# Kernel tuning notes

Measured on AMD Instinct MI355X. Metric: run time of the kernel, lower is better.

Reference implementation:

```python
import jax, jax.numpy as jnp
import numpy as np

FACTOR = 5

def _prob_attention(queries, keys, values):
    # queries/keys/values: [B, L, H, D]
    B, L_Q, H, D = queries.shape
    L_K = keys.shape[1]
    q = jnp.transpose(queries, (0, 2, 1, 3))  # [B,H,L_Q,D]
    k = jnp.transpose(keys, (0, 2, 1, 3))
    v = jnp.transpose(values, (0, 2, 1, 3))

    U_part = min(FACTOR * int(np.ceil(np.log(L_K))), L_K)  # sample_k
    u = min(FACTOR * int(np.ceil(np.log(L_Q))), L_Q)       # n_top

    # random K sampling (fixed key -> deterministic reference)
    skey = jax.random.key(42)
    index_sample = jax.random.randint(skey, (L_Q, U_part), 0, L_K)  # [L_Q, S]
    K_sample = k[:, :, index_sample, :]  # [B,H,L_Q,S,D]
    Q_K_sample = jnp.einsum('bhqd,bhqsd->bhqs', q, K_sample)  # [B,H,L_Q,S]

    # sparsity measure and top-u query selection
    M = jnp.max(Q_K_sample, axis=-1) - jnp.mean(Q_K_sample, axis=-1)  # [B,H,L_Q]
    _, M_top = jax.lax.top_k(M, u)  # [B,H,u]

    Q_reduce = jnp.take_along_axis(q, M_top[..., None], axis=2)  # [B,H,u,D]
    scores = jnp.einsum('bhud,bhkd->bhuk', Q_reduce, k)  # [B,H,u,L_K]
    scale = 1.0 / jnp.sqrt(jnp.asarray(D, dtype=q.dtype))
    scores = scores * scale

    # initial context: mean of V over keys, tiled over queries (mask_flag=False)
    V_mean = jnp.mean(v, axis=-2, keepdims=True)  # [B,H,1,D]
    context = jnp.broadcast_to(V_mean, (B, H, L_Q, D))

    attn = jax.nn.softmax(scores, axis=-1)  # [B,H,u,L_K]
    update = jnp.einsum('bhuk,bhkd->bhud', attn, v)  # [B,H,u,D]

    # scatter updates into context at selected query positions
    bi = jnp.arange(B)[:, None, None]
    hi = jnp.arange(H)[None, :, None]
    context = context.at[bi, hi, M_top].set(update)

    return jnp.transpose(context, (0, 2, 1, 3))  # [B,L_Q,H,D]


def setup_inputs() -> dict:
    key = jax.random.key(0)
    kq, kk, kv = jax.random.split(key, 3)
    B, L, H, D = 4, 2048, 8, 64
    return {
        'queries': jax.random.normal(kq, (B, L, H, D), dtype=jnp.float32),
        'keys': jax.random.normal(kk, (B, L, H, D), dtype=jnp.float32),
        'values': jax.random.normal(kv, (B, L, H, D), dtype=jnp.float32),
        'attn_mask': jnp.zeros((1,), dtype=jnp.bool_),  # unused (mask_flag=False)
    }


def reference(queries, keys, values, attn_mask):
    context = _prob_attention(queries, keys, values)
    return context
```

## Files before the change

kernel.cpp:

```cpp
#include <hip/hip_runtime.h>
#include <hip/hip_bf16.h>
#include <math.h>
#include <stdint.h>

static constexpr int BB = 4;
static constexpr int LL = 2048;
static constexpr int HH = 8;
static constexpr int DD = 64;
static constexpr int UU = 40;
static constexpr int NSAMP = 40;
static constexpr int BHL = BB * HH * LL;
static constexpr int NIDX = LL * NSAMP;
static constexpr int ROWSTRIDE = HH * DD;
static constexpr int VCHUNKS = 64;
static constexpr int NC = 16;
static constexpr int CROWS = LL / NC;
static constexpr int NBLK = BB * HH * NC;

static constexpr size_t WS_NEED = 5420032;

__device__ __forceinline__ uint32_t rotl32(uint32_t x, uint32_t n) {
  return (x << n) | (x >> (32u - n));
}

__device__ __forceinline__ void tf2x32(uint32_t k0, uint32_t k1,
                                       uint32_t x0, uint32_t x1,
                                       uint32_t& o0, uint32_t& o1) {
  uint32_t ks[3] = {k0, k1, k0 ^ k1 ^ 0x1BD11BDAu};
  x0 += ks[0];
  x1 += ks[1];
  const uint32_t rotA[4] = {13u, 15u, 26u, 6u};
  const uint32_t rotB[4] = {17u, 29u, 16u, 24u};
#pragma unroll
  for (int i = 0; i < 5; ++i) {
    const uint32_t* r = (i & 1) ? rotB : rotA;
#pragma unroll
    for (int j = 0; j < 4; ++j) {
      x0 += x1;
      x1 = rotl32(x1, r[j]);
      x1 ^= x0;
    }
    x0 += ks[(i + 1) % 3];
    x1 += ks[(i + 2) % 3] + (uint32_t)(i + 1);
  }
  o0 = x0;
  o1 = x1;
}

__global__ void k_build_idx(int* __restrict__ idx) {
  int i = blockIdx.x * 256 + threadIdx.x;
  if (i >= NIDX) return;
  uint32_t ka, kb;
  tf2x32(0u, 42u, 0u, 1u, ka, kb);
  uint32_t o0, o1;
  tf2x32(ka, kb, 0u, (uint32_t)i, o0, o1);
  idx[i] = (int)((o0 ^ o1) & 2047u);
}

__device__ __forceinline__ float dot4(float4 a, float4 b) {
  return a.x * b.x + a.y * b.y + a.z * b.z + a.w * b.w;
}

__global__ void k_scores_M(const float* __restrict__ q, const float* __restrict__ k,
                           const int* __restrict__ idx, float* __restrict__ M) {
  int w = (blockIdx.x * blockDim.x + threadIdx.x) >> 6;
  int lane = threadIdx.x & 63;
  if (w >= BHL) return;
  int qq = w & (LL - 1);
  int h = (w >> 11) & (HH - 1);
  int b = w >> 14;
  int rr = lane >> 3;
  int dc = lane & 7;
  const float* qrow = q + (((size_t)b * LL + qq) * HH + h) * DD;
  float4 q0 = ((const float4*)qrow)[dc * 2];
  float4 q1 = ((const float4*)qrow)[dc * 2 + 1];
  const float* kbase = k + ((size_t)b * LL * HH + h) * DD;
  const int* ridx = idx + qq * NSAMP;
  int kr[5];
#pragma unroll
  for (int it = 0; it < 5; ++it) kr[it] = ridx[it * 8 + rr];
  float mx = -1.0e30f, sm = 0.0f;
#pragma unroll
  for (int it = 0; it < 5; ++it) {
    const float4* kp = (const float4*)(kbase + (size_t)kr[it] * ROWSTRIDE);
    float p = dot4(q0, kp[dc * 2]) + dot4(q1, kp[dc * 2 + 1]);
    p += __shfl_xor(p, 1);
    p += __shfl_xor(p, 2);
    p += __shfl_xor(p, 4);
    mx = fmaxf(mx, p);
    sm += p;
  }
#pragma unroll
  for (int off = 8; off <= 32; off <<= 1) {
    mx = fmaxf(mx, __shfl_xor(mx, off));
    sm += __shfl_xor(sm, off);
  }
  if (lane == 0) M[w] = mx - sm * (1.0f / (float)NSAMP);
}

__global__ void k_topk(const float* __restrict__ M, int* __restrict__ mtop) {
  __shared__ uint32_t keys[LL];
  __shared__ int hist[256];
  __shared__ int scan_res[2];
  __shared__ int nsel, neq;
  __shared__ int sel[UU];
  __shared__ int eqlist[64];
  int bh = blockIdx.x;
  int t = threadIdx.x;
  const float* m = M + (size_t)bh * LL;
  for (int i = t; i < LL; i += 256) {
    uint32_t u = __float_as_uint(m[i]);
    keys[i] = (u & 0x80000000u) ? ~u : (u | 0x80000000u);
  }
  if (t == 0) { nsel = 0; neq = 0; }
  __syncthreads();

  uint32_t prefix = 0, prefmask = 0;
  int remaining = UU;
#pragma unroll
  for (int shift = 24; shift >= 0; shift -= 8) {
    hist[t] = 0;
    __syncthreads();
    for (int i = t; i < LL; i += 256) {
      uint32_t kk = keys[i];
      if ((kk & prefmask) == prefix) atomicAdd(&hist[(kk >> shift) & 0xFF], 1);
    }
    __syncthreads();
    if (t < 64) {
      int b0 = t * 4;
      int c0 = hist[b0], c1 = hist[b0 + 1], c2 = hist[b0 + 2], c3 = hist[b0 + 3];
      int g = c0 + c1 + c2 + c3;
      int s = g;
#pragma unroll
      for (int off = 1; off < 64; off <<= 1) {
        int o = __shfl_down(s, off);
        if (t + off < 64) s += o;
      }
      int a3 = s - g;
      int a2 = a3 + c3;
      int a1 = a2 + c2;
      int a0 = a1 + c1;
      if (a3 < remaining && remaining <= a3 + c3) { scan_res[0] = b0 + 3; scan_res[1] = a3; }
      if (a2 < remaining && remaining <= a2 + c2) { scan_res[0] = b0 + 2; scan_res[1] = a2; }
      if (a1 < remaining && remaining <= a1 + c1) { scan_res[0] = b0 + 1; scan_res[1] = a1; }
      if (a0 < remaining && remaining <= a0 + c0) { scan_res[0] = b0 + 0; scan_res[1] = a0; }
    }
    __syncthreads();
    prefix |= ((uint32_t)scan_res[0] << shift);
    prefmask |= (0xFFu << shift);
    remaining -= scan_res[1];
    __syncthreads();
  }

  uint32_t T = prefix;
  for (int i = t; i < LL; i += 256) {
    uint32_t kk = keys[i];
    if (kk > T) {
      int p = atomicAdd(&nsel, 1);
      sel[p] = i;
    } else if (kk == T) {
      int p = atomicAdd(&neq, 1);
      if (p < 64) eqlist[p] = i;
    }
  }
  __syncthreads();
  if (t == 0) {
    int need = UU - nsel;
    int count = neq < 64 ? neq : 64;
    for (int r = 0; r < need; ++r) {
      int mn = 1 << 30, mpos = 0;
      for (int e = 0; e < count; ++e)
        if (eqlist[e] < mn) { mn = eqlist[e]; mpos = e; }
      sel[nsel + r] = mn;
      eqlist[mpos] = 1 << 30;
    }
  }
  __syncthreads();
  if (t < UU) mtop[bh * UU + t] = sel[t];
}

__global__ void k_vmean_part(const float* __restrict__ v, float* __restrict__ partial) {
  __shared__ float part[4][DD];
  int bid = blockIdx.x;
  int bh = bid >> 6;
  int chunk = bid & 63;
  int b = bh >> 3, h = bh & 7;
  int t = threadIdx.x;
  int wv = t >> 6, lane = t & 63;
  int l0 = chunk * (LL / VCHUNKS);
  const float* base = v + ((size_t)b * LL * HH + h) * DD + lane;
  float s = 0.0f;
#pragma unroll
  for (int r = wv; r < LL / VCHUNKS; r += 4) s += base[(size_t)(l0 + r) * ROWSTRIDE];
  part[wv][lane] = s;
  __syncthreads();
  if (t < DD) {
    partial[(size_t)bid * DD + t] =
        (part[0][t] + part[1][t]) + (part[2][t] + part[3][t]);
  }
}

__global__ void k_vmean_final(const float* __restrict__ partial, float* __restrict__ vmean) {
  int bh = blockIdx.x;
  int d = threadIdx.x;
  const float* p = partial + (size_t)bh * VCHUNKS * DD + d;
  float s = 0.0f;
#pragma unroll
  for (int c = 0; c < VCHUNKS; ++c) s += p[(size_t)c * DD];
  vmean[bh * DD + d] = s * (1.0f / (float)LL);
}

__global__ void k_fill(const float* __restrict__ vmean, float* __restrict__ out) {
  int f = blockIdx.x * 256 + threadIdx.x;
  int d4 = f & 15;
  int h = (f >> 4) & 7;
  int b = f >> 18;
  ((float4*)out)[f] = ((const float4*)vmean)[(((b << 3) + h) << 4) + d4];
}

__global__ void __launch_bounds__(256)
k_attn_part(const float* __restrict__ q, const float* __restrict__ k,
            const float* __restrict__ v, const int* __restrict__ mtop,
            float* __restrict__ pm, float* __restrict__ ps,
            float* __restrict__ pacc) {
  __shared__ float qs[UU][DD];
  __shared__ float sc[UU][CROWS];
  int blk = blockIdx.x;
  int c = blk & (NC - 1);
  int bh = blk >> 4;
  int b = bh >> 3, h = bh & 7;
  int t = threadIdx.x;
  int wv = t >> 6, lane = t & 63;
  int l0 = c * CROWS;

  for (int i = t; i < UU * DD; i += 256) {
    int j = i >> 6, d = i & 63;
    int l = mtop[bh * UU + j];
    qs[j][d] = q[(((size_t)b * LL + l) * HH + h) * DD + d];
  }
  __syncthreads();

  const float* kbase = k + ((size_t)b * LL * HH + h) * DD;

  int rr = lane & 15, dcq = lane >> 4;
  float4 kv0[4], kv1[4];
  {
    const float* kr0 = kbase + (size_t)(l0 + wv * 32 + rr) * ROWSTRIDE + dcq * 16;
    const float* kr1 = kbase + (size_t)(l0 + wv * 32 + 16 + rr) * ROWSTRIDE + dcq * 16;
#pragma unroll
    for (int i = 0; i < 4; ++i) {
      kv0[i] = *(const float4*)(kr0 + i * 4);
      kv1[i] = *(const float4*)(kr1 + i * 4);
    }
  }
#pragma unroll 4
  for (int j = 0; j < UU; ++j) {
    const float* qp = &qs[j][dcq * 16];
    float4 qa = *(const float4*)(qp);
    float4 qb = *(const float4*)(qp + 4);
    float4 qc = *(const float4*)(qp + 8);
    float4 qd = *(const float4*)(qp + 12);
    float p0 = dot4(qa, kv0[0]) + dot4(qb, kv0[1]) + dot4(qc, kv0[2]) + dot4(qd, kv0[3]);
    float p1 = dot4(qa, kv1[0]) + dot4(qb, kv1[1]) + dot4(qc, kv1[2]) + dot4(qd, kv1[3]);
    p0 += __shfl_xor(p0, 16);
    p0 += __shfl_xor(p0, 32);
    p1 += __shfl_xor(p1, 16);
    p1 += __shfl_xor(p1, 32);
    if (lane < 16) {
      sc[j][wv * 32 + lane] = p0 * 0.125f;
      sc[j][wv * 32 + 16 + lane] = p1 * 0.125f;
    }
  }
  __syncthreads();

#pragma unroll
  for (int jj = 0; jj < 10; ++jj) {
    int j = wv * 10 + jj;
    float a0 = sc[j][lane];
    float a1 = sc[j][lane + 64];
    float mx = fmaxf(a0, a1);
#pragma unroll
    for (int off = 32; off; off >>= 1) mx = fmaxf(mx, __shfl_xor(mx, off));
    float e0 = expf(a0 - mx), e1 = expf(a1 - mx);
    sc[j][lane] = e0;
    sc[j][lane + 64] = e1;
    float s = e0 + e1;
#pragma unroll
    for (int off = 32; off; off >>= 1) s += __shfl_xor(s, off);
    if (lane == 0) {
      pm[(size_t)blk * UU + j] = mx;
      ps[(size_t)blk * UU + j] = s;
    }
  }

  const float* vbase = v + ((size_t)b * LL * HH + h) * DD + lane;
  float acc[10];
#pragma unroll
  for (int jj = 0; jj < 10; ++jj) acc[jj] = 0.0f;
  for (int r = 0; r < CROWS; r += 4) {
    float v0 = vbase[(size_t)(l0 + r + 0) * ROWSTRIDE];
    float v1 = vbase[(size_t)(l0 + r + 1) * ROWSTRIDE];
    float v2 = vbase[(size_t)(l0 + r + 2) * ROWSTRIDE];
    float v3 = vbase[(size_t)(l0 + r + 3) * ROWSTRIDE];
#pragma unroll
    for (int jj = 0; jj < 10; ++jj) {
      int j = wv * 10 + jj;
      float4 p4 = *(const float4*)&sc[j][r];
      acc[jj] += p4.x * v0 + p4.y * v1 + p4.z * v2 + p4.w * v3;
    }
  }
#pragma unroll
  for (int jj = 0; jj < 10; ++jj) {
    int j = wv * 10 + jj;
    pacc[((size_t)blk * UU + j) * DD + lane] = acc[jj];
  }
}

__global__ void k_attn_comb(const float* __restrict__ pm, const float* __restrict__ ps,
                            const float* __restrict__ pacc, const int* __restrict__ mtop,
                            float* __restrict__ out) {
  int wid = (blockIdx.x * 256 + threadIdx.x) >> 6;
  int lane = threadIdx.x & 63;
  if (wid >= BB * HH * UU) return;
  int j = wid % UU;
  int bh = wid / UU;
  int b = bh >> 3, h = bh & 7;
  float mv = (lane < NC) ? pm[((size_t)(bh * NC + lane)) * UU + j] : -1.0e30f;
  float mx = mv;
#pragma unroll
  for (int off = 8; off; off >>= 1) mx = fmaxf(mx, __shfl_xor(mx, off));
  mx = __shfl(mx, 0);
  float e = (lane < NC) ? expf(mv - mx) : 0.0f;
  float sv = (lane < NC) ? ps[((size_t)(bh * NC + lane)) * UU + j] * e : 0.0f;
  float st = sv;
#pragma unroll
  for (int off = 8; off; off >>= 1) st += __shfl_xor(st, off);
  st = __shfl(st, 0);
  float a = 0.0f;
#pragma unroll
  for (int c = 0; c < NC; ++c) {
    float ec = __shfl(e, c);
    a += ec * pacc[((size_t)(bh * NC + c) * UU + j) * DD + lane];
  }
  int l = mtop[bh * UU + j];
  out[(((size_t)b * LL + l) * HH + h) * DD + lane] = a / st;
}

__global__ void k_attn_mono(const float* __restrict__ q, const float* __restrict__ k,
                            const float* __restrict__ v, const int* __restrict__ mtop,
                            float* __restrict__ out) {
  __shared__ float sc[LL];
  __shared__ float redm[4];
  __shared__ float reds[4];
  __shared__ float redp[4][DD];
  int blk = blockIdx.x;
  int j = blk % UU;
  int bh = blk / UU;
  int b = bh >> 3, h = bh & 7;
  int l = mtop[bh * UU + j];
  int t = threadIdx.x;
  int wv = t >> 6, lane = t & 63;
  int dc = t & 15, r2 = (t >> 4) & 3;
  const float4* qrow = (const float4*)(q + (((size_t)b * LL + l) * HH + h) * DD);
  float4 qv = qrow[dc];
  const float* kbase = k + ((size_t)b * LL * HH + h) * DD;
#pragma unroll 4
  for (int base = wv * 4; base < LL; base += 16) {
    int row = base + r2;
    const float4* krow = (const float4*)(kbase + (size_t)row * ROWSTRIDE);
    float4 kv = krow[dc];
    float p = dot4(qv, kv);
    p += __shfl_xor(p, 1);
    p += __shfl_xor(p, 2);
    p += __shfl_xor(p, 4);
    p += __shfl_xor(p, 8);
    if (dc == 0) sc[row] = p * 0.125f;
  }
  __syncthreads();
  const float4* sc4 = (const float4*)sc;
  float4 ea0 = sc4[t];
  float4 ea1 = sc4[t + 256];
  float mx = fmaxf(fmaxf(fmaxf(ea0.x, ea0.y), fmaxf(ea0.z, ea0.w)),
                   fmaxf(fmaxf(ea1.x, ea1.y), fmaxf(ea1.z, ea1.w)));
#pragma unroll
  for (int off = 32; off; off >>= 1) mx = fmaxf(mx, __shfl_xor(mx, off));
  if (lane == 0) redm[wv] = mx;
  __syncthreads();
  mx = fmaxf(fmaxf(redm[0], redm[1]), fmaxf(redm[2], redm[3]));
  ea0.x = expf(ea0.x - mx); ea0.y = expf(ea0.y - mx);
  ea0.z = expf(ea0.z - mx); ea0.w = expf(ea0.w - mx);
  ea1.x = expf(ea1.x - mx); ea1.y = expf(ea1.y - mx);
  ea1.z = expf(ea1.z - mx); ea1.w = expf(ea1.w - mx);
  float psum = ((ea0.x + ea0.y) + (ea0.z + ea0.w)) + ((ea1.x + ea1.y) + (ea1.z + ea1.w));
  float4* sc4w = (float4*)sc;
  sc4w[t] = ea0;
  sc4w[t + 256] = ea1;
#pragma unroll
  for (int off = 32; off; off >>= 1) psum += __shfl_xor(psum, off);
  if (lane == 0) reds[wv] = psum;
  __syncthreads();
  float inv = 1.0f / ((reds[0] + reds[1]) + (reds[2] + reds[3]));
  const float* vbase = v + ((size_t)b * LL * HH + h) * DD + lane;
  float acc = 0.0f;
#pragma unroll 2
  for (int base = wv * 4; base < LL; base += 16) {
    float4 p4 = sc4[base >> 2];
    acc += p4.x * vbase[(size_t)(base + 0) * ROWSTRIDE];
    acc += p4.y * vbase[(size_t)(base + 1) * ROWSTRIDE];
    acc += p4.z * vbase[(size_t)(base + 2) * ROWSTRIDE];
    acc += p4.w * vbase[(size_t)(base + 3) * ROWSTRIDE];
  }
  redp[wv][lane] = acc;
  __syncthreads();
  if (t < DD) {
    float r = (redp[0][t] + redp[1][t]) + (redp[2][t] + redp[3][t]);
    out[(((size_t)b * LL + l) * HH + h) * DD + t] = r * inv;
  }
}

extern "C" void kernel_launch(void* const* d_in, const int* in_sizes, int n_in,
                              void* d_out, int out_size, void* d_ws, size_t ws_size,
                              hipStream_t stream) {
  const float* q = (const float*)d_in[0];
  const float* k = (const float*)d_in[1];
  const float* v = (const float*)d_in[2];
  float* out = (float*)d_out;
  char* ws = (char*)d_ws;
  bool big = ws_size >= WS_NEED;

  if (big) {
    float* pm = (float*)(ws);
    float* ps = (float*)(ws + 81920);
    float* pacc = (float*)(ws + 163840);
    float* M = (float*)(ws);
    int* idx = (int*)(ws + 262144);
    float* vpart = (float*)(ws);
    int* mtop = (int*)(ws + 5406720);
    float* vmean = (float*)(ws + 5411840);

    k_build_idx<<<(NIDX + 255) / 256, 256, 0, stream>>>(idx);
    k_scores_M<<<BHL / 4, 256, 0, stream>>>(q, k, idx, M);
    k_topk<<<BB * HH, 256, 0, stream>>>(M, mtop);
    k_vmean_part<<<BB * HH * VCHUNKS, 256, 0, stream>>>(v, vpart);
    k_vmean_final<<<BB * HH, DD, 0, stream>>>(vpart, vmean);
    k_fill<<<(BB * LL * HH * DD / 4) / 256, 256, 0, stream>>>(vmean, out);
    k_attn_part<<<NBLK, 256, 0, stream>>>(q, k, v, mtop, pm, ps, pacc);
    k_attn_comb<<<(BB * HH * UU * 64) / 256, 256, 0, stream>>>(pm, ps, pacc, mtop, out);
  } else {
    float* M = (float*)(ws);
    int* idx = (int*)(ws + 262144);
    int* mtop = (int*)(ws + 589824);
    float* vmean = (float*)(ws + 594944);
    float* vpart = (float*)(ws);

    k_build_idx<<<(NIDX + 255) / 256, 256, 0, stream>>>(idx);
    k_scores_M<<<BHL / 4, 256, 0, stream>>>(q, k, idx, M);
    k_topk<<<BB * HH, 256, 0, stream>>>(M, mtop);
    k_vmean_part<<<BB * HH * VCHUNKS, 256, 0, stream>>>(v, vpart);
    k_vmean_final<<<BB * HH, DD, 0, stream>>>(vpart, vmean);
    k_fill<<<(BB * LL * HH * DD / 4) / 256, 256, 0, stream>>>(vmean, out);
    k_attn_mono<<<BB * HH * UU, 256, 0, stream>>>(q, k, v, mtop, out);
  }
}
```

Before: 178.6 us.

## Fuse random index generation into sampling kernel and double attention key split

The Threefry index generation moves into k_scores_M, with each lane computing one sample index that is then shuffled across the wave. This removes a separate launch and the idx buffer round-trip. Blocks in k_scores_M are also remapped in a strided order. The split-K attention now uses 32 chunks of 64 keys instead of 16 chunks of 128, giving more blocks at the cost of more partials to combine. The workspace requirement roughly doubles, so the big path depends on the workspace size provided.

```diff
diff --git a/kernel.cpp b/kernel.cpp
--- a/kernel.cpp
+++ b/kernel.cpp
@@ -10,14 +10,13 @@
 static constexpr int UU = 40;
 static constexpr int NSAMP = 40;
 static constexpr int BHL = BB * HH * LL;
-static constexpr int NIDX = LL * NSAMP;
 static constexpr int ROWSTRIDE = HH * DD;
 static constexpr int VCHUNKS = 64;
-static constexpr int NC = 16;
+static constexpr int NC = 32;
 static constexpr int CROWS = LL / NC;
 static constexpr int NBLK = BB * HH * NC;
 
-static constexpr size_t WS_NEED = 5420032;
+static constexpr size_t WS_NEED = 10826752;
 
 __device__ __forceinline__ uint32_t rotl32(uint32_t x, uint32_t n) {
   return (x << n) | (x >> (32u - n));
@@ -47,38 +46,35 @@
   o1 = x1;
 }
 
-__global__ void k_build_idx(int* __restrict__ idx) {
-  int i = blockIdx.x * 256 + threadIdx.x;
-  if (i >= NIDX) return;
+__device__ __forceinline__ float dot4(float4 a, float4 b) {
+  return a.x * b.x + a.y * b.y + a.z * b.z + a.w * b.w;
+}
+
+__global__ void k_scores_M(const float* __restrict__ q, const float* __restrict__ k,
+                           float* __restrict__ M) {
+  const int NWG = BHL / 4;
+  int wg = (blockIdx.x & 7) * (NWG / 8) + (blockIdx.x >> 3);
+  int w = wg * 4 + (threadIdx.x >> 6);
+  int lane = threadIdx.x & 63;
+  int qq = w & (LL - 1);
+  int h = (w >> 11) & (HH - 1);
+  int b = w >> 14;
+
   uint32_t ka, kb;
   tf2x32(0u, 42u, 0u, 1u, ka, kb);
   uint32_t o0, o1;
-  tf2x32(ka, kb, 0u, (uint32_t)i, o0, o1);
-  idx[i] = (int)((o0 ^ o1) & 2047u);
-}
-
-__device__ __forceinline__ float dot4(float4 a, float4 b) {
-  return a.x * b.x + a.y * b.y + a.z * b.z + a.w * b.w;
-}
-
-__global__ void k_scores_M(const float* __restrict__ q, const float* __restrict__ k,
-                           const int* __restrict__ idx, float* __restrict__ M) {
-  int w = (blockIdx.x * blockDim.x + threadIdx.x) >> 6;
-  int lane = threadIdx.x & 63;
-  if (w >= BHL) return;
-  int qq = w & (LL - 1);
-  int h = (w >> 11) & (HH - 1);
-  int b = w >> 14;
+  tf2x32(ka, kb, 0u, (uint32_t)(qq * NSAMP + lane), o0, o1);
+  int idxv = (int)((o0 ^ o1) & 2047u);
+
   int rr = lane >> 3;
   int dc = lane & 7;
   const float* qrow = q + (((size_t)b * LL + qq) * HH + h) * DD;
   float4 q0 = ((const float4*)qrow)[dc * 2];
   float4 q1 = ((const float4*)qrow)[dc * 2 + 1];
   const float* kbase = k + ((size_t)b * LL * HH + h) * DD;
-  const int* ridx = idx + qq * NSAMP;
   int kr[5];
 #pragma unroll
-  for (int it = 0; it < 5; ++it) kr[it] = ridx[it * 8 + rr];
+  for (int it = 0; it < 5; ++it) kr[it] = __shfl(idxv, it * 8 + rr);
   float mx = -1.0e30f, sm = 0.0f;
 #pragma unroll
   for (int it = 0; it < 5; ++it) {
@@ -227,7 +223,7 @@
   __shared__ float sc[UU][CROWS];
   int blk = blockIdx.x;
   int c = blk & (NC - 1);
-  int bh = blk >> 4;
+  int bh = blk >> 5;
   int b = bh >> 3, h = bh & 7;
   int t = threadIdx.x;
   int wv = t >> 6, lane = t & 63;
@@ -243,15 +239,11 @@
   const float* kbase = k + ((size_t)b * LL * HH + h) * DD;
 
   int rr = lane & 15, dcq = lane >> 4;
-  float4 kv0[4], kv1[4];
+  float4 kv0[4];
   {
-    const float* kr0 = kbase + (size_t)(l0 + wv * 32 + rr) * ROWSTRIDE + dcq * 16;
-    const float* kr1 = kbase + (size_t)(l0 + wv * 32 + 16 + rr) * ROWSTRIDE + dcq * 16;
-#pragma unroll
-    for (int i = 0; i < 4; ++i) {
-      kv0[i] = *(const float4*)(kr0 + i * 4);
-      kv1[i] = *(const float4*)(kr1 + i * 4);
-    }
+    const float* kr0 = kbase + (size_t)(l0 + wv * 16 + rr) * ROWSTRIDE + dcq * 16;
+#pragma unroll
+    for (int i = 0; i < 4; ++i) kv0[i] = *(const float4*)(kr0 + i * 4);
   }
 #pragma unroll 4
   for (int j = 0; j < UU; ++j) {
@@ -261,15 +253,9 @@
     float4 qc = *(const float4*)(qp + 8);
     float4 qd = *(const float4*)(qp + 12);
     float p0 = dot4(qa, kv0[0]) + dot4(qb, kv0[1]) + dot4(qc, kv0[2]) + dot4(qd, kv0[3]);
-    float p1 = dot4(qa, kv1[0]) + dot4(qb, kv1[1]) + dot4(qc, kv1[2]) + dot4(qd, kv1[3]);
     p0 += __shfl_xor(p0, 16);
     p0 += __shfl_xor(p0, 32);
-    p1 += __shfl_xor(p1, 16);
-    p1 += __shfl_xor(p1, 32);
-    if (lane < 16) {
-      sc[j][wv * 32 + lane] = p0 * 0.125f;
-      sc[j][wv * 32 + 16 + lane] = p1 * 0.125f;
-    }
+    if (lane < 16) sc[j][wv * 16 + lane] = p0 * 0.125f;
   }
   __syncthreads();
 
@@ -277,14 +263,12 @@
   for (int jj = 0; jj < 10; ++jj) {
     int j = wv * 10 + jj;
     float a0 = sc[j][lane];
-    float a1 = sc[j][lane + 64];
-    float mx = fmaxf(a0, a1);
+    float mx = a0;
 #pragma unroll
     for (int off = 32; off; off >>= 1) mx = fmaxf(mx, __shfl_xor(mx, off));
-    float e0 = expf(a0 - mx), e1 = expf(a1 - mx);
+    float e0 = expf(a0 - mx);
     sc[j][lane] = e0;
-    sc[j][lane + 64] = e1;
-    float s = e0 + e1;
+    float s = e0;
 #pragma unroll
     for (int off = 32; off; off >>= 1) s += __shfl_xor(s, off);
     if (lane == 0) {
@@ -328,13 +312,13 @@
   float mv = (lane < NC) ? pm[((size_t)(bh * NC + lane)) * UU + j] : -1.0e30f;
   float mx = mv;
 #pragma unroll
-  for (int off = 8; off; off >>= 1) mx = fmaxf(mx, __shfl_xor(mx, off));
+  for (int off = 16; off; off >>= 1) mx = fmaxf(mx, __shfl_xor(mx, off));
   mx = __shfl(mx, 0);
   float e = (lane < NC) ? expf(mv - mx) : 0.0f;
   float sv = (lane < NC) ? ps[((size_t)(bh * NC + lane)) * UU + j] * e : 0.0f;
   float st = sv;
 #pragma unroll
-  for (int off = 8; off; off >>= 1) st += __shfl_xor(st, off);
+  for (int off = 16; off; off >>= 1) st += __shfl_xor(st, off);
   st = __shfl(st, 0);
   float a = 0.0f;
 #pragma unroll
@@ -430,16 +414,14 @@
 
   if (big) {
     float* pm = (float*)(ws);
-    float* ps = (float*)(ws + 81920);
-    float* pacc = (float*)(ws + 163840);
+    float* ps = (float*)(ws + 163840);
+    float* pacc = (float*)(ws + 327680);
     float* M = (float*)(ws);
-    int* idx = (int*)(ws + 262144);
     float* vpart = (float*)(ws);
-    int* mtop = (int*)(ws + 5406720);
-    float* vmean = (float*)(ws + 5411840);
-
-    k_build_idx<<<(NIDX + 255) / 256, 256, 0, stream>>>(idx);
-    k_scores_M<<<BHL / 4, 256, 0, stream>>>(q, k, idx, M);
+    int* mtop = (int*)(ws + 10813440);
+    float* vmean = (float*)(ws + 10818560);
+
+    k_scores_M<<<BHL / 4, 256, 0, stream>>>(q, k, M);
     k_topk<<<BB * HH, 256, 0, stream>>>(M, mtop);
     k_vmean_part<<<BB * HH * VCHUNKS, 256, 0, stream>>>(v, vpart);
     k_vmean_final<<<BB * HH, DD, 0, stream>>>(vpart, vmean);
@@ -448,13 +430,11 @@
     k_attn_comb<<<(BB * HH * UU * 64) / 256, 256, 0, stream>>>(pm, ps, pacc, mtop, out);
   } else {
     float* M = (float*)(ws);
-    int* idx = (int*)(ws + 262144);
-    int* mtop = (int*)(ws + 589824);
-    float* vmean = (float*)(ws + 594944);
     float* vpart = (float*)(ws);
-
-    k_build_idx<<<(NIDX + 255) / 256, 256, 0, stream>>>(idx);
-    k_scores_M<<<BHL / 4, 256, 0, stream>>>(q, k, idx, M);
+    int* mtop = (int*)(ws + 524288);
+    float* vmean = (float*)(ws + 529408);
+
+    k_scores_M<<<BHL / 4, 256, 0, stream>>>(q, k, M);
     k_topk<<<BB * HH, 256, 0, stream>>>(M, mtop);
     k_vmean_part<<<BB * HH * VCHUNKS, 256, 0, stream>>>(v, vpart);
     k_vmean_final<<<BB * HH, DD, 0, stream>>>(vpart, vmean);
```

Result: no change. 177.2 us (-0.8%).

## Fuse pipeline into four kernels with inline index RNG and lookup-table output

Applied to the files above, without the earlier changes.

The sample-index generation is computed inline in the scoring kernel, with indices shared through wave shuffles and K loads batched ahead of the math. The V partial means are produced in the same launch as scoring. Top-k and the final V-mean reduction share one launch, and top-k also writes a per-position lookup table. The attention partial kernel is split into two query halves to double block count. The fill and combine kernels become a single output kernel that writes either the V mean or the combined attention row per position. This cuts launch count and the extra full-output write pass. The cost is redundant threefry work per wave and extra table memory traffic.

```diff
diff --git a/kernel.cpp b/kernel.cpp
--- a/kernel.cpp
+++ b/kernel.cpp
@@ -10,14 +10,15 @@
 static constexpr int UU = 40;
 static constexpr int NSAMP = 40;
 static constexpr int BHL = BB * HH * LL;
-static constexpr int NIDX = LL * NSAMP;
 static constexpr int ROWSTRIDE = HH * DD;
 static constexpr int VCHUNKS = 64;
 static constexpr int NC = 16;
-static constexpr int CROWS = LL / NC;
-static constexpr int NBLK = BB * HH * NC;
-
-static constexpr size_t WS_NEED = 5420032;
+static constexpr int CR = 128;
+static constexpr int QS = 20;
+static constexpr int SCOREBLK = BHL / 4;
+static constexpr int P1BLK = SCOREBLK + BB * HH * VCHUNKS;
+
+static constexpr size_t WS_NEED = 5682176;
 
 __device__ __forceinline__ uint32_t rotl32(uint32_t x, uint32_t n) {
   return (x << n) | (x >> (32u - n));
@@ -47,175 +48,177 @@
   o1 = x1;
 }
 
-__global__ void k_build_idx(int* __restrict__ idx) {
-  int i = blockIdx.x * 256 + threadIdx.x;
-  if (i >= NIDX) return;
-  uint32_t ka, kb;
-  tf2x32(0u, 42u, 0u, 1u, ka, kb);
-  uint32_t o0, o1;
-  tf2x32(ka, kb, 0u, (uint32_t)i, o0, o1);
-  idx[i] = (int)((o0 ^ o1) & 2047u);
-}
-
 __device__ __forceinline__ float dot4(float4 a, float4 b) {
   return a.x * b.x + a.y * b.y + a.z * b.z + a.w * b.w;
 }
 
-__global__ void k_scores_M(const float* __restrict__ q, const float* __restrict__ k,
-                           const int* __restrict__ idx, float* __restrict__ M) {
-  int w = (blockIdx.x * blockDim.x + threadIdx.x) >> 6;
-  int lane = threadIdx.x & 63;
-  if (w >= BHL) return;
-  int qq = w & (LL - 1);
-  int h = (w >> 11) & (HH - 1);
-  int b = w >> 14;
-  int rr = lane >> 3;
-  int dc = lane & 7;
-  const float* qrow = q + (((size_t)b * LL + qq) * HH + h) * DD;
-  float4 q0 = ((const float4*)qrow)[dc * 2];
-  float4 q1 = ((const float4*)qrow)[dc * 2 + 1];
-  const float* kbase = k + ((size_t)b * LL * HH + h) * DD;
-  const int* ridx = idx + qq * NSAMP;
-  int kr[5];
-#pragma unroll
-  for (int it = 0; it < 5; ++it) kr[it] = ridx[it * 8 + rr];
-  float mx = -1.0e30f, sm = 0.0f;
-#pragma unroll
-  for (int it = 0; it < 5; ++it) {
-    const float4* kp = (const float4*)(kbase + (size_t)kr[it] * ROWSTRIDE);
-    float p = dot4(q0, kp[dc * 2]) + dot4(q1, kp[dc * 2 + 1]);
-    p += __shfl_xor(p, 1);
-    p += __shfl_xor(p, 2);
-    p += __shfl_xor(p, 4);
-    mx = fmaxf(mx, p);
-    sm += p;
-  }
-#pragma unroll
-  for (int off = 8; off <= 32; off <<= 1) {
-    mx = fmaxf(mx, __shfl_xor(mx, off));
-    sm += __shfl_xor(sm, off);
-  }
-  if (lane == 0) M[w] = mx - sm * (1.0f / (float)NSAMP);
-}
-
-__global__ void k_topk(const float* __restrict__ M, int* __restrict__ mtop) {
-  __shared__ uint32_t keys[LL];
-  __shared__ int hist[256];
-  __shared__ int scan_res[2];
-  __shared__ int nsel, neq;
-  __shared__ int sel[UU];
-  __shared__ int eqlist[64];
-  int bh = blockIdx.x;
-  int t = threadIdx.x;
-  const float* m = M + (size_t)bh * LL;
-  for (int i = t; i < LL; i += 256) {
-    uint32_t u = __float_as_uint(m[i]);
-    keys[i] = (u & 0x80000000u) ? ~u : (u | 0x80000000u);
-  }
-  if (t == 0) { nsel = 0; neq = 0; }
-  __syncthreads();
-
-  uint32_t prefix = 0, prefmask = 0;
-  int remaining = UU;
-#pragma unroll
-  for (int shift = 24; shift >= 0; shift -= 8) {
-    hist[t] = 0;
+__global__ void __launch_bounds__(256)
+k_phase1(const float* __restrict__ q, const float* __restrict__ k,
+         const float* __restrict__ v, float* __restrict__ M,
+         float* __restrict__ vpart) {
+  if (blockIdx.x < SCOREBLK) {
+    int wg = (blockIdx.x & 7) * (SCOREBLK / 8) + (blockIdx.x >> 3);
+    int w = wg * 4 + (threadIdx.x >> 6);
+    int lane = threadIdx.x & 63;
+    int qq = w & (LL - 1);
+    int h = (w >> 11) & (HH - 1);
+    int b = w >> 14;
+    uint32_t ka, kb;
+    tf2x32(0u, 42u, 0u, 1u, ka, kb);
+    uint32_t o0, o1;
+    tf2x32(ka, kb, 0u, (uint32_t)(qq * NSAMP + lane), o0, o1);
+    int idxv = (int)((o0 ^ o1) & 2047u);
+    int rr = lane >> 3;
+    int dc = lane & 7;
+    const float* qrow = q + (((size_t)b * LL + qq) * HH + h) * DD;
+    float4 q0 = ((const float4*)qrow)[dc * 2];
+    float4 q1 = ((const float4*)qrow)[dc * 2 + 1];
+    const float* kbase = k + ((size_t)b * LL * HH + h) * DD;
+    int kr[5];
+#pragma unroll
+    for (int it = 0; it < 5; ++it) kr[it] = __shfl(idxv, it * 8 + rr);
+    float4 kva[5], kvb[5];
+#pragma unroll
+    for (int it = 0; it < 5; ++it) {
+      const float4* kp = (const float4*)(kbase + (size_t)kr[it] * ROWSTRIDE);
+      kva[it] = kp[dc * 2];
+      kvb[it] = kp[dc * 2 + 1];
+    }
+    float mx = -1.0e30f, sm = 0.0f;
+#pragma unroll
+    for (int it = 0; it < 5; ++it) {
+      float p = dot4(q0, kva[it]) + dot4(q1, kvb[it]);
+      p += __shfl_xor(p, 1);
+      p += __shfl_xor(p, 2);
+      p += __shfl_xor(p, 4);
+      mx = fmaxf(mx, p);
+      sm += p;
+    }
+#pragma unroll
+    for (int off = 8; off <= 32; off <<= 1) {
+      mx = fmaxf(mx, __shfl_xor(mx, off));
+      sm += __shfl_xor(sm, off);
+    }
+    if (lane == 0) M[w] = mx - sm * (1.0f / (float)NSAMP);
+  } else {
+    __shared__ float part[4][DD];
+    int bid = blockIdx.x - SCOREBLK;
+    int bh = bid >> 6;
+    int chunk = bid & 63;
+    int b = bh >> 3, h = bh & 7;
+    int t = threadIdx.x;
+    int wv = t >> 6, lane = t & 63;
+    int l0 = chunk * (LL / VCHUNKS);
+    const float* base = v + ((size_t)b * LL * HH + h) * DD + lane;
+    float s = 0.0f;
+#pragma unroll
+    for (int r = wv; r < LL / VCHUNKS; r += 4) s += base[(size_t)(l0 + r) * ROWSTRIDE];
+    part[wv][lane] = s;
     __syncthreads();
+    if (t < DD) {
+      vpart[(size_t)bid * DD + t] =
+          (part[0][t] + part[1][t]) + (part[2][t] + part[3][t]);
+    }
+  }
+}
+
+__global__ void __launch_bounds__(256)
+k_phase2(const float* __restrict__ M, const float* __restrict__ vpart,
+         int* __restrict__ mtop, float* __restrict__ vmean, int* __restrict__ tbl) {
+  if (blockIdx.x < BB * HH) {
+    __shared__ uint32_t keys[LL];
+    __shared__ int hist[256];
+    __shared__ int scan_res[2];
+    __shared__ int nsel, neq;
+    __shared__ int sel[UU];
+    __shared__ int eqlist[64];
+    int bh = blockIdx.x;
+    int t = threadIdx.x;
+    const float* m = M + (size_t)bh * LL;
+    for (int i = t; i < LL; i += 256) {
+      uint32_t u = __float_as_uint(m[i]);
+      keys[i] = (u & 0x80000000u) ? ~u : (u | 0x80000000u);
+      tbl[bh * LL + i] = -1;
+    }
+    if (t == 0) { nsel = 0; neq = 0; }
+    __syncthreads();
+
+    uint32_t prefix = 0, prefmask = 0;
+    int remaining = UU;
+#pragma unroll
+    for (int shift = 24; shift >= 0; shift -= 8) {
+      hist[t] = 0;
+      __syncthreads();
+      for (int i = t; i < LL; i += 256) {
+        uint32_t kk = keys[i];
+        if ((kk & prefmask) == prefix) atomicAdd(&hist[(kk >> shift) & 0xFF], 1);
+      }
+      __syncthreads();
+      if (t < 64) {
+        int b0 = t * 4;
+        int c0 = hist[b0], c1 = hist[b0 + 1], c2 = hist[b0 + 2], c3 = hist[b0 + 3];
+        int g = c0 + c1 + c2 + c3;
+        int s = g;
+#pragma unroll
+        for (int off = 1; off < 64; off <<= 1) {
+          int o = __shfl_down(s, off);
+          if (t + off < 64) s += o;
+        }
+        int a3 = s - g;
+        int a2 = a3 + c3;
+        int a1 = a2 + c2;
+        int a0 = a1 + c1;
+        if (a3 < remaining && remaining <= a3 + c3) { scan_res[0] = b0 + 3; scan_res[1] = a3; }
+        if (a2 < remaining && remaining <= a2 + c2) { scan_res[0] = b0 + 2; scan_res[1] = a2; }
+        if (a1 < remaining && remaining <= a1 + c1) { scan_res[0] = b0 + 1; scan_res[1] = a1; }
+        if (a0 < remaining && remaining <= a0 + c0) { scan_res[0] = b0 + 0; scan_res[1] = a0; }
+      }
+      __syncthreads();
+      prefix |= ((uint32_t)scan_res[0] << shift);
+      prefmask |= (0xFFu << shift);
+      remaining -= scan_res[1];
+      __syncthreads();
+    }
+
+    uint32_t T = prefix;
     for (int i = t; i < LL; i += 256) {
       uint32_t kk = keys[i];
-      if ((kk & prefmask) == prefix) atomicAdd(&hist[(kk >> shift) & 0xFF], 1);
+      if (kk > T) {
+        int p = atomicAdd(&nsel, 1);
+        sel[p] = i;
+      } else if (kk == T) {
+        int p = atomicAdd(&neq, 1);
+        if (p < 64) eqlist[p] = i;
+      }
     }
     __syncthreads();
-    if (t < 64) {
-      int b0 = t * 4;
-      int c0 = hist[b0], c1 = hist[b0 + 1], c2 = hist[b0 + 2], c3 = hist[b0 + 3];
-      int g = c0 + c1 + c2 + c3;
-      int s = g;
-#pragma unroll
-      for (int off = 1; off < 64; off <<= 1) {
-        int o = __shfl_down(s, off);
-        if (t + off < 64) s += o;
+    if (t == 0) {
+      int need = UU - nsel;
+      int count = neq < 64 ? neq : 64;
+      for (int r = 0; r < need; ++r) {
+        int mn = 1 << 30, mpos = 0;
+        for (int e = 0; e < count; ++e)
+          if (eqlist[e] < mn) { mn = eqlist[e]; mpos = e; }
+        sel[nsel + r] = mn;
+        eqlist[mpos] = 1 << 30;
       }
-      int a3 = s - g;
-      int a2 = a3 + c3;
-      int a1 = a2 + c2;
-      int a0 = a1 + c1;
-      if (a3 < remaining && remaining <= a3 + c3) { scan_res[0] = b0 + 3; scan_res[1] = a3; }
-      if (a2 < remaining && remaining <= a2 + c2) { scan_res[0] = b0 + 2; scan_res[1] = a2; }
-      if (a1 < remaining && remaining <= a1 + c1) { scan_res[0] = b0 + 1; scan_res[1] = a1; }
-      if (a0 < remaining && remaining <= a0 + c0) { scan_res[0] = b0 + 0; scan_res[1] = a0; }
     }
     __syncthreads();
-    prefix |= ((uint32_t)scan_res[0] << shift);
-    prefmask |= (0xFFu << shift);
-    remaining -= scan_res[1];
-    __syncthreads();
-  }
-
-  uint32_t T = prefix;
-  for (int i = t; i < LL; i += 256) {
-    uint32_t kk = keys[i];
-    if (kk > T) {
-      int p = atomicAdd(&nsel, 1);
-      sel[p] = i;
-    } else if (kk == T) {
-      int p = atomicAdd(&neq, 1);
-      if (p < 64) eqlist[p] = i;
-    }
-  }
-  __syncthreads();
-  if (t == 0) {
-    int need = UU - nsel;
-    int count = neq < 64 ? neq : 64;
-    for (int r = 0; r < need; ++r) {
-      int mn = 1 << 30, mpos = 0;
-      for (int e = 0; e < count; ++e)
-        if (eqlist[e] < mn) { mn = eqlist[e]; mpos = e; }
-      sel[nsel + r] = mn;
-      eqlist[mpos] = 1 << 30;
-    }
-  }
-  __syncthreads();
-  if (t < UU) mtop[bh * UU + t] = sel[t];
-}
-
-__global__ void k_vmean_part(const float* __restrict__ v, float* __restrict__ partial) {
-  __shared__ float part[4][DD];
-  int bid = blockIdx.x;
-  int bh = bid >> 6;
-  int chunk = bid & 63;
-  int b = bh >> 3, h = bh & 7;
-  int t = threadIdx.x;
-  int wv = t >> 6, lane = t & 63;
-  int l0 = chunk * (LL / VCHUNKS);
-  const float* base = v + ((size_t)b * LL * HH + h) * DD + lane;
-  float s = 0.0f;
-#pragma unroll
-  for (int r = wv; r < LL / VCHUNKS; r += 4) s += base[(size_t)(l0 + r) * ROWSTRIDE];
-  part[wv][lane] = s;
-  __syncthreads();
-  if (t < DD) {
-    partial[(size_t)bid * DD + t] =
-        (part[0][t] + part[1][t]) + (part[2][t] + part[3][t]);
-  }
-}
-
-__global__ void k_vmean_final(const float* __restrict__ partial, float* __restrict__ vmean) {
-  int bh = blockIdx.x;
-  int d = threadIdx.x;
-  const float* p = partial + (size_t)bh * VCHUNKS * DD + d;
-  float s = 0.0f;
-#pragma unroll
-  for (int c = 0; c < VCHUNKS; ++c) s += p[(size_t)c * DD];
-  vmean[bh * DD + d] = s * (1.0f / (float)LL);
-}
-
-__global__ void k_fill(const float* __restrict__ vmean, float* __restrict__ out) {
-  int f = blockIdx.x * 256 + threadIdx.x;
-  int d4 = f & 15;
-  int h = (f >> 4) & 7;
-  int b = f >> 18;
-  ((float4*)out)[f] = ((const float4*)vmean)[(((b << 3) + h) << 4) + d4];
+    if (t < UU) {
+      mtop[bh * UU + t] = sel[t];
+      tbl[bh * LL + sel[t]] = t;
+    }
+  } else {
+    int bh = blockIdx.x - BB * HH;
+    int d = threadIdx.x;
+    if (d < DD) {
+      const float* p = vpart + (size_t)bh * VCHUNKS * DD + d;
+      float s = 0.0f;
+#pragma unroll
+      for (int c = 0; c < VCHUNKS; ++c) s += p[(size_t)c * DD];
+      vmean[bh * DD + d] = s * (1.0f / (float)LL);
+    }
+  }
 }
 
 __global__ void __launch_bounds__(256)
@@ -223,25 +226,26 @@
             const float* __restrict__ v, const int* __restrict__ mtop,
             float* __restrict__ pm, float* __restrict__ ps,
             float* __restrict__ pacc) {
-  __shared__ float qs[UU][DD];
-  __shared__ float sc[UU][CROWS];
+  __shared__ float qs_[QS][DD];
+  __shared__ float sc[QS][CR];
   int blk = blockIdx.x;
   int c = blk & (NC - 1);
-  int bh = blk >> 4;
+  int qh = (blk >> 4) & 1;
+  int bh = blk >> 5;
   int b = bh >> 3, h = bh & 7;
   int t = threadIdx.x;
   int wv = t >> 6, lane = t & 63;
-  int l0 = c * CROWS;
-
-  for (int i = t; i < UU * DD; i += 256) {
-    int j = i >> 6, d = i & 63;
-    int l = mtop[bh * UU + j];
-    qs[j][d] = q[(((size_t)b * LL + l) * HH + h) * DD + d];
+  int l0 = c * CR;
+  int j0 = qh * QS;
+
+  for (int i = t; i < QS * DD; i += 256) {
+    int jj = i >> 6, d = i & 63;
+    int l = mtop[bh * UU + j0 + jj];
+    qs_[jj][d] = q[(((size_t)b * LL + l) * HH + h) * DD + d];
   }
   __syncthreads();
 
   const float* kbase = k + ((size_t)b * LL * HH + h) * DD;
-
   int rr = lane & 15, dcq = lane >> 4;
   float4 kv0[4], kv1[4];
   {
@@ -254,8 +258,8 @@
     }
   }
 #pragma unroll 4
-  for (int j = 0; j < UU; ++j) {
-    const float* qp = &qs[j][dcq * 16];
+  for (int jj = 0; jj < QS; ++jj) {
+    const float* qp = &qs_[jj][dcq * 16];
     float4 qa = *(const float4*)(qp);
     float4 qb = *(const float4*)(qp + 4);
     float4 qc = *(const float4*)(qp + 8);
@@ -267,83 +271,89 @@
     p1 += __shfl_xor(p1, 16);
     p1 += __shfl_xor(p1, 32);
     if (lane < 16) {
-      sc[j][wv * 32 + lane] = p0 * 0.125f;
-      sc[j][wv * 32 + 16 + lane] = p1 * 0.125f;
-    }
-  }
-  __syncthreads();
-
-#pragma unroll
-  for (int jj = 0; jj < 10; ++jj) {
-    int j = wv * 10 + jj;
-    float a0 = sc[j][lane];
-    float a1 = sc[j][lane + 64];
+      sc[jj][wv * 32 + lane] = p0 * 0.125f;
+      sc[jj][wv * 32 + 16 + lane] = p1 * 0.125f;
+    }
+  }
+  __syncthreads();
+
+#pragma unroll
+  for (int u = 0; u < 5; ++u) {
+    int jj = wv * 5 + u;
+    float a0 = sc[jj][lane];
+    float a1 = sc[jj][lane + 64];
     float mx = fmaxf(a0, a1);
 #pragma unroll
     for (int off = 32; off; off >>= 1) mx = fmaxf(mx, __shfl_xor(mx, off));
     float e0 = expf(a0 - mx), e1 = expf(a1 - mx);
-    sc[j][lane] = e0;
-    sc[j][lane + 64] = e1;
+    sc[jj][lane] = e0;
+    sc[jj][lane + 64] = e1;
     float s = e0 + e1;
 #pragma unroll
     for (int off = 32; off; off >>= 1) s += __shfl_xor(s, off);
     if (lane == 0) {
-      pm[(size_t)blk * UU + j] = mx;
-      ps[(size_t)blk * UU + j] = s;
-    }
-  }
-
+      pm[(size_t)(bh * NC + c) * UU + j0 + jj] = mx;
+      ps[(size_t)(bh * NC + c) * UU + j0 + jj] = s;
+    }
+  }
   const float* vbase = v + ((size_t)b * LL * HH + h) * DD + lane;
-  float acc[10];
-#pragma unroll
-  for (int jj = 0; jj < 10; ++jj) acc[jj] = 0.0f;
-  for (int r = 0; r < CROWS; r += 4) {
+  float acc[5] = {0.f, 0.f, 0.f, 0.f, 0.f};
+  for (int r = 0; r < CR; r += 4) {
     float v0 = vbase[(size_t)(l0 + r + 0) * ROWSTRIDE];
     float v1 = vbase[(size_t)(l0 + r + 1) * ROWSTRIDE];
     float v2 = vbase[(size_t)(l0 + r + 2) * ROWSTRIDE];
     float v3 = vbase[(size_t)(l0 + r + 3) * ROWSTRIDE];
 #pragma unroll
-    for (int jj = 0; jj < 10; ++jj) {
-      int j = wv * 10 + jj;
-      float4 p4 = *(const float4*)&sc[j][r];
-      acc[jj] += p4.x * v0 + p4.y * v1 + p4.z * v2 + p4.w * v3;
-    }
-  }
-#pragma unroll
-  for (int jj = 0; jj < 10; ++jj) {
-    int j = wv * 10 + jj;
-    pacc[((size_t)blk * UU + j) * DD + lane] = acc[jj];
-  }
-}
-
-__global__ void k_attn_comb(const float* __restrict__ pm, const float* __restrict__ ps,
-                            const float* __restrict__ pacc, const int* __restrict__ mtop,
-                            float* __restrict__ out) {
+    for (int u = 0; u < 5; ++u) {
+      float4 p4 = *(const float4*)&sc[wv * 5 + u][r];
+      acc[u] += p4.x * v0 + p4.y * v1 + p4.z * v2 + p4.w * v3;
+    }
+  }
+#pragma unroll
+  for (int u = 0; u < 5; ++u) {
+    pacc[((size_t)(bh * NC + c) * UU + j0 + wv * 5 + u) * DD + lane] = acc[u];
+  }
+}
+
+__global__ void __launch_bounds__(256)
+k_out(const float* __restrict__ pm, const float* __restrict__ ps,
+      const float* __restrict__ pacc, const int* __restrict__ tbl,
+      const float* __restrict__ vmean, float* __restrict__ out) {
   int wid = (blockIdx.x * 256 + threadIdx.x) >> 6;
   int lane = threadIdx.x & 63;
-  if (wid >= BB * HH * UU) return;
-  int j = wid % UU;
-  int bh = wid / UU;
+  int l = wid & (LL - 1);
+  int bh = wid >> 11;
   int b = bh >> 3, h = bh & 7;
-  float mv = (lane < NC) ? pm[((size_t)(bh * NC + lane)) * UU + j] : -1.0e30f;
-  float mx = mv;
-#pragma unroll
-  for (int off = 8; off; off >>= 1) mx = fmaxf(mx, __shfl_xor(mx, off));
-  mx = __shfl(mx, 0);
-  float e = (lane < NC) ? expf(mv - mx) : 0.0f;
-  float sv = (lane < NC) ? ps[((size_t)(bh * NC + lane)) * UU + j] * e : 0.0f;
-  float st = sv;
-#pragma unroll
-  for (int off = 8; off; off >>= 1) st += __shfl_xor(st, off);
-  st = __shfl(st, 0);
-  float a = 0.0f;
-#pragma unroll
-  for (int c = 0; c < NC; ++c) {
-    float ec = __shfl(e, c);
-    a += ec * pacc[((size_t)(bh * NC + c) * UU + j) * DD + lane];
-  }
-  int l = mtop[bh * UU + j];
-  out[(((size_t)b * LL + l) * HH + h) * DD + lane] = a / st;
+  int j = tbl[bh * LL + l];
+  float* orow = out + (((size_t)b * LL + l) * HH + h) * DD;
+  if (j < 0) {
+    orow[lane] = vmean[bh * DD + lane];
+  } else {
+    float mv = (lane < NC) ? pm[(size_t)(bh * NC + lane) * UU + j] : -1.0e30f;
+    float mx = mv;
+#pragma unroll
+    for (int off = 32; off; off >>= 1) mx = fmaxf(mx, __shfl_xor(mx, off));
+    float e = (lane < NC) ? expf(mv - mx) : 0.0f;
+    float sv = (lane < NC) ? ps[(size_t)(bh * NC + lane) * UU + j] * e : 0.0f;
+    float st = sv;
+#pragma unroll
+    for (int off = 32; off; off >>= 1) st += __shfl_xor(st, off);
+    float a = 0.0f;
+#pragma unroll
+    for (int c2 = 0; c2 < NC; ++c2) {
+      float ec = __shfl(e, c2);
+      a += ec * pacc[((size_t)(bh * NC + c2) * UU + j) * DD + lane];
+    }
+    orow[lane] = a / st;
+  }
+}
+
+__global__ void k_fill(const float* __restrict__ vmean, float* __restrict__ out) {
+  int f = blockIdx.x * 256 + threadIdx.x;
+  int d4 = f & 15;
+  int h = (f >> 4) & 7;
+  int b = f >> 18;
+  ((float4*)out)[f] = ((const float4*)vmean)[(((b << 3) + h) << 4) + d4];
 }
 
 __global__ void k_attn_mono(const float* __restrict__ q, const float* __restrict__ k,
@@ -426,38 +436,30 @@
   const float* v = (const float*)d_in[2];
   float* out = (float*)d_out;
   char* ws = (char*)d_ws;
-  bool big = ws_size >= WS_NEED;
-
-  if (big) {
+
+  if (ws_size >= WS_NEED) {
+    float* M = (float*)(ws);
+    float* vpart = (float*)(ws + 262144);
     float* pm = (float*)(ws);
     float* ps = (float*)(ws + 81920);
     float* pacc = (float*)(ws + 163840);
-    float* M = (float*)(ws);
-    int* idx = (int*)(ws + 262144);
-    float* vpart = (float*)(ws);
     int* mtop = (int*)(ws + 5406720);
     float* vmean = (float*)(ws + 5411840);
-
-    k_build_idx<<<(NIDX + 255) / 256, 256, 0, stream>>>(idx);
-    k_scores_M<<<BHL / 4, 256, 0, stream>>>(q, k, idx, M);
-    k_topk<<<BB * HH, 256, 0, stream>>>(M, mtop);
-    k_vmean_part<<<BB * HH * VCHUNKS, 256, 0, stream>>>(v, vpart);
-    k_vmean_final<<<BB * HH, DD, 0, stream>>>(vpart, vmean);
-    k_fill<<<(BB * LL * HH * DD / 4) / 256, 256, 0, stream>>>(vmean, out);
-    k_attn_part<<<NBLK, 256, 0, stream>>>(q, k, v, mtop, pm, ps, pacc);
-    k_attn_comb<<<(BB * HH * UU * 64) / 256, 256, 0, stream>>>(pm, ps, pacc, mtop, out);
+    int* tbl = (int*)(ws + 5420032);
+
+    k_phase1<<<P1BLK, 256, 0, stream>>>(q, k, v, M, vpart);
+    k_phase2<<<2 * BB * HH, 256, 0, stream>>>(M, vpart, mtop, vmean, tbl);
+    k_attn_part<<<BB * HH * NC * 2, 256, 0, stream>>>(q, k, v, mtop, pm, ps, pacc);
+    k_out<<<BHL / 4, 256, 0, stream>>>(pm, ps, pacc, tbl, vmean, out);
   } else {
     float* M = (float*)(ws);
-    int* idx = (int*)(ws + 262144);
-    int* mtop = (int*)(ws + 589824);
-    float* vmean = (float*)(ws + 594944);
-    float* vpart = (float*)(ws);
-
-    k_build_idx<<<(NIDX + 255) / 256, 256, 0, stream>>>(idx);
-    k_scores_M<<<BHL / 4, 256, 0, stream>>>(q, k, idx, M);
-    k_topk<<<BB * HH, 256, 0, stream>>>(M, mtop);
-    k_vmean_part<<<BB * HH * VCHUNKS, 256, 0, stream>>>(v, vpart);
-    k_vmean_final<<<BB * HH, DD, 0, stream>>>(vpart, vmean);
+    int* tbl = (int*)(ws);
+    float* vpart = (float*)(ws + 262144);
+    int* mtop = (int*)(ws + 786432);
+    float* vmean = (float*)(ws + 791552);
+
+    k_phase1<<<P1BLK, 256, 0, stream>>>(q, k, v, M, vpart);
+    k_phase2<<<2 * BB * HH, 256, 0, stream>>>(M, vpart, mtop, vmean, tbl);
     k_fill<<<(BB * LL * HH * DD / 4) / 256, 256, 0, stream>>>(vmean, out);
     k_attn_mono<<<BB * HH * UU, 256, 0, stream>>>(q, k, v, mtop, out);
   }
```

Result: faster. 170.7 us (-4.4%).
